# Performance work log

Hardware: AMD Instinct MI355X
Metric: run time of the kernel (lower is better)

Reference implementation:

```python
import jax, jax.numpy as jnp
import numpy as np

V = 20000; FV = 2000; PV = 31
SE = 400; FE = 50; PE = 5; NE = 5
FR = FE + PE + NE  # 60, field_rep_embed_size
H = 512; HH = H // 2  # decoder hidden, encoder per-direction hidden
B = 32; T = 32; S = 100
TE = 300  # target_lookup dim (hardcoded in module)


def setup_inputs() -> dict:
    key = jax.random.key(0)
    ks = jax.random.split(key, 26)
    g = lambda k, shape, s: (jax.random.normal(k, shape, jnp.float32) * s)
    inp = {}
    inp['sent'] = jax.random.randint(ks[0], (B, T), 0, V)
    inp['value'] = jax.random.randint(ks[1], (B, S), 0, V)
    inp['field'] = jax.random.randint(ks[2], (B, S), 0, FV)
    inp['ppos'] = jax.random.randint(ks[3], (B, S), 0, PV)
    inp['pneg'] = jax.random.randint(ks[4], (B, S), 0, PV)
    inp['batch_size'] = B
    inp['value_mask'] = jnp.ones((B, S), jnp.float32)
    inp['align_prob'] = jax.random.uniform(ks[5], (B, S, V), jnp.float32)
    # embedding tables
    inp['sent_emb'] = g(ks[6], (V, SE), 0.05)
    inp['field_emb'] = g(ks[7], (FV, FE), 0.05)
    inp['ppos_emb'] = g(ks[8], (PV, PE), 0.05)
    inp['pneg_emb'] = g(ks[9], (PV, NE), 0.05)
    inp['target_emb'] = g(ks[10], (V, TE), 0.05)
    # bidirectional encoder LSTM (per-direction hidden HH), torch gate order i,f,g,o
    ein = SE + FR
    inp['Wi_f'] = g(ks[11], (ein, 4 * HH), ein ** -0.5)
    inp['Wh_f'] = g(ks[12], (HH, 4 * HH), HH ** -0.5)
    inp['b_f'] = jnp.zeros((4 * HH,), jnp.float32)
    inp['Wi_b'] = g(ks[13], (ein, 4 * HH), ein ** -0.5)
    inp['Wh_b'] = g(ks[14], (HH, 4 * HH), HH ** -0.5)
    inp['b_b'] = jnp.zeros((4 * HH,), jnp.float32)
    # decoder LSTM cell + dual attention params
    inp['Wi_d'] = g(ks[15], (SE, 4 * H), SE ** -0.5)
    inp['Wh_d'] = g(ks[16], (H, 4 * H), H ** -0.5)
    inp['b_d'] = jnp.zeros((4 * H,), jnp.float32)
    inp['Wa'] = g(ks[17], (H, H), H ** -0.5)   # encoder-state attention proj
    inp['Wf'] = g(ks[18], (FR, H), FR ** -0.5) # field-rep attention proj
    inp['Wo'] = g(ks[19], (2 * H, H), (2 * H) ** -0.5)  # output proj [h;ctx]
    inp['Wl'] = g(ks[20], (2 * H + SE, 1), (2 * H + SE) ** -0.5)  # lamda gate
    inp['bl'] = jnp.zeros((1,), jnp.float32)
    # linear_out: encoder_hidden_size -> vocab
    inp['Wout'] = g(ks[21], (H, V), H ** -0.5)
    inp['bout'] = jnp.zeros((V,), jnp.float32)
    return inp


def _cell(x, h, c, Wi, Wh, b):
    z = x @ Wi + h @ Wh + b
    i, f, g, o = jnp.split(z, 4, axis=-1)
    c = jax.nn.sigmoid(f) * c + jax.nn.sigmoid(i) * jnp.tanh(g)
    h = jax.nn.sigmoid(o) * jnp.tanh(c)
    return h, c


def _run_lstm(xseq, Wi, Wh, b):
    # xseq [B,L,E] -> hs [B,L,Hn], (hT, cT)
    Bn = xseq.shape[0]; Hn = Wh.shape[0]
    init = (jnp.zeros((Bn, Hn), xseq.dtype), jnp.zeros((Bn, Hn), xseq.dtype))
    def step(carry, xt):
        h, c = _cell(xt, carry[0], carry[1], Wi, Wh, b)
        return (h, c), h
    (hT, cT), hs = jax.lax.scan(step, init, jnp.swapaxes(xseq, 0, 1))
    return jnp.swapaxes(hs, 0, 1), hT, cT


def reference(sent, value, field, ppos, pneg, batch_size, value_mask, align_prob,
              sent_emb, field_emb, ppos_emb, pneg_emb, target_emb,
              Wi_f, Wh_f, b_f, Wi_b, Wh_b, b_b,
              Wi_d, Wh_d, b_d, Wa, Wf, Wo, Wl, bl, Wout, bout):
    # --- encoder input: word emb of table values + field/pos/neg-pos embs ---
    input_d = sent_emb[value]                                     # [B,S,SE]
    input_z = jnp.concatenate([field_emb[field], ppos_emb[ppos], pneg_emb[pneg]], axis=2)  # [B,S,FR]
    enc_in = jnp.concatenate([input_d, input_z], axis=2)          # [B,S,SE+FR]
    # bidirectional LSTM (dropout is eval-mode identity)
    hs_f, hTf, cTf = _run_lstm(enc_in, Wi_f, Wh_f, b_f)
    hs_b, hTb, cTb = _run_lstm(enc_in[:, ::-1], Wi_b, Wh_b, b_b)
    enc_out = jnp.concatenate([hs_f, hs_b[:, ::-1]], axis=-1)     # [B,S,H]
    h0 = jnp.concatenate([hTf, hTb], axis=-1)                     # [B,H]
    c0 = jnp.concatenate([cTf, cTb], axis=-1)

    # --- dual-attention decoder ---
    x_seq = sent_emb[sent]                                        # [B,T,SE]
    enc_proj = jnp.einsum('bsh,hk->bsk', enc_out, Wa)             # word-level keys
    z_proj = jnp.einsum('bsf,fk->bsk', input_z, Wf)               # field-level keys

    def dstep(carry, xt):
        h, c = _cell(xt, carry[0], carry[1], Wi_d, Wh_d, b_d)
        alpha = jax.nn.softmax(jnp.einsum('bsh,bh->bs', enc_proj, h), axis=-1)
        beta = jax.nn.softmax(jnp.einsum('bsh,bh->bs', z_proj, h), axis=-1)
        g = alpha * beta
        g = g / (jnp.sum(g, axis=-1, keepdims=True) + 1e-9)       # dual attn weights
        ctx = jnp.einsum('bs,bsh->bh', g, enc_out)
        out = jnp.tanh(jnp.concatenate([h, ctx], axis=-1) @ Wo)   # [B,H]
        lam = jax.nn.sigmoid(jnp.concatenate([h, ctx, xt], axis=-1) @ Wl + bl)  # [B,1]
        return (h, c), (out, g, lam)

    (hT, cT), (outs, attn, lam) = jax.lax.scan(dstep, (h0, c0), jnp.swapaxes(x_seq, 0, 1))
    outs = jnp.swapaxes(outs, 0, 1)   # [B,T,H]
    attn = jnp.swapaxes(attn, 0, 1)   # [B,T,S]
    lam = jnp.swapaxes(lam, 0, 1)     # [B,T,1]

    p_mod = jax.nn.log_softmax(outs @ Wout + bout, axis=2)        # [B,T,V]
    p_lex = jnp.einsum('bts,bsv->btv', attn, align_prob)          # bmm
    p_bias = jax.nn.log_softmax(lam * p_lex + (1.0 - lam) * p_mod, axis=2)

    # position_idx_to_value: vectorized gather replacing the scalar double loop
    max_idx_attn = jnp.argmax(attn, axis=2)                       # [B,T]
    word_idx = jnp.take_along_axis(value, max_idx_attn, axis=1)   # [B,T]
    attn_pred = target_emb[word_idx]                              # [B,T,300]
    decoder_pred = target_emb[jnp.argmax(p_bias, axis=2)]         # [B,T,300]
    return p_bias, (hT, cT), attn_pred, decoder_pred
```

## Files before the change

### kernel.cpp

```cpp
#include <hip/hip_runtime.h>
#include <cstdint>
#include <cstddef>

static constexpr int Bn  = 32;
static constexpr int Tn  = 32;
static constexpr int Sn  = 100;
static constexpr int Vn  = 20000;
static constexpr int SEn = 400;
static constexpr int EINn= 460;
static constexpr int Hn  = 512;
static constexpr int HHn = 256;
static constexpr int TEn = 300;

__device__ __forceinline__ float sigm(float x) { return 1.f / (1.f + expf(-x)); }

__device__ __forceinline__ void fma4(float hk, const float4 w,
                                     float& zi, float& zf, float& zg, float& zo) {
    zi = fmaf(hk, w.x, zi); zf = fmaf(hk, w.y, zf);
    zg = fmaf(hk, w.z, zg); zo = fmaf(hk, w.w, zo);
}

__global__ __launch_bounds__(256) void embed_kernel(
    const int* __restrict__ value, const int* __restrict__ field,
    const int* __restrict__ ppos, const int* __restrict__ pneg,
    const int* __restrict__ sent,
    const float* __restrict__ sent_emb, const float* __restrict__ field_emb,
    const float* __restrict__ ppos_emb, const float* __restrict__ pneg_emb,
    float* __restrict__ enc_in, float* __restrict__ x_seq)
{
    int i = blockIdx.x * 256 + threadIdx.x;
    const int total1 = Bn * Sn * EINn;
    if (i < total1) {
        int e = i % EINn, bs = i / EINn;
        float v;
        if (e < SEn)      v = sent_emb[(size_t)value[bs] * SEn + e];
        else if (e < 450) v = field_emb[field[bs] * 50 + (e - 400)];
        else if (e < 455) v = ppos_emb[ppos[bs] * 5 + (e - 450)];
        else              v = pneg_emb[pneg[bs] * 5 + (e - 455)];
        enc_in[i] = v;
    } else {
        int i2 = i - total1;
        if (i2 < Bn * Tn * SEn) {
            int e = i2 % SEn, bt = i2 / SEn;
            x_seq[i2] = sent_emb[(size_t)sent[bt] * SEn + e];
        }
    }
}

__global__ __launch_bounds__(256) void transpose_wh_kernel(
    const float* __restrict__ Whf, const float* __restrict__ Whb,
    const float* __restrict__ Whd,
    float* __restrict__ Whf_t, float* __restrict__ Whb_t, float* __restrict__ Whd_t)
{
    int i = blockIdx.x * 256 + threadIdx.x;
    if (i < 65536) {
        int k = i >> 8, u = i & 255;
        const float* p = Whf + (size_t)k * 1024 + u;
        float4 o;
        o.x = p[0]; o.y = p[256]; o.z = p[512]; o.w = p[768];
        *(float4*)(Whf_t + (size_t)i * 4) = o;
        p = Whb + (size_t)k * 1024 + u;
        o.x = p[0]; o.y = p[256]; o.z = p[512]; o.w = p[768];
        *(float4*)(Whb_t + (size_t)i * 4) = o;
    } else {
        int j = i - 65536;
        if (j < 262144) {
            int k = j >> 9, u = j & 511;
            const float* p = Whd + (size_t)k * 2048 + u;
            float4 o;
            o.x = p[0]; o.y = p[512]; o.z = p[1024]; o.w = p[1536];
            *(float4*)(Whd_t + (size_t)j * 4) = o;
        }
    }
}

__global__ __launch_bounds__(256) void gemm128_kernel(
    const float* __restrict__ A, const float* __restrict__ Bm,
    const float* __restrict__ bias, float* __restrict__ C,
    int M, int N, int K, int lda, int ldb, int ldc)
{
    __shared__ float As[8][128];
    __shared__ float Bs[8][128];
    const int bm = blockIdx.y * 128, bn = blockIdx.x * 128;
    const int tid = threadIdx.x;
    const int tx = tid & 15, ty = tid >> 4;
    const int row0 = ty * 8, col0 = tx * 8;
    float acc[8][8] = {};
    for (int k0 = 0; k0 < K; k0 += 8) {
        #pragma unroll
        for (int i = 0; i < 4; ++i) {
            int idx = tid + 256 * i;
            int m = idx >> 3, kk = idx & 7;
            float v = 0.f;
            if (bm + m < M && k0 + kk < K) v = A[(size_t)(bm + m) * lda + (k0 + kk)];
            As[kk][m] = v;
        }
        #pragma unroll
        for (int i = 0; i < 4; ++i) {
            int idx = tid + 256 * i;
            int kk = idx >> 7, n = idx & 127;
            float v = 0.f;
            if (k0 + kk < K && bn + n < N) v = Bm[(size_t)(k0 + kk) * ldb + (bn + n)];
            Bs[kk][n] = v;
        }
        __syncthreads();
        #pragma unroll
        for (int kk = 0; kk < 8; ++kk) {
            float a[8], b[8];
            #pragma unroll
            for (int i = 0; i < 8; ++i) a[i] = As[kk][row0 + i];
            #pragma unroll
            for (int j = 0; j < 8; ++j) b[j] = Bs[kk][col0 + j];
            #pragma unroll
            for (int i = 0; i < 8; ++i)
                #pragma unroll
                for (int j = 0; j < 8; ++j) acc[i][j] = fmaf(a[i], b[j], acc[i][j]);
        }
        __syncthreads();
    }
    #pragma unroll
    for (int i = 0; i < 8; ++i) {
        int m = bm + row0 + i;
        if (m >= M) continue;
        #pragma unroll
        for (int j = 0; j < 8; ++j) {
            int n = bn + col0 + j;
            if (n < N) {
                float v = acc[i][j];
                if (bias) v += bias[n];
                C[(size_t)m * ldc + n] = v;
            }
        }
    }
}

__global__ __launch_bounds__(256) void enc_lstm2_kernel(
    const float* __restrict__ Xf, const float* __restrict__ Xb,
    const float4* __restrict__ Whf_t, const float4* __restrict__ Whb_t,
    float* __restrict__ enc_out, float* __restrict__ h0, float* __restrict__ c0)
{
    const int b = blockIdx.x >> 1, dir = blockIdx.x & 1;
    const float* __restrict__ X = dir ? Xb : Xf;
    const float4* __restrict__ W = dir ? Whb_t : Whf_t;
    __shared__ __align__(16) float h_sh[HHn];
    const int u = threadIdx.x;
    float c = 0.f;
    h_sh[u] = 0.f;
    __syncthreads();
    for (int step = 0; step < Sn; ++step) {
        const int s = dir ? (Sn - 1 - step) : step;
        const float* xr = X + ((size_t)(b * Sn + s)) * 1024;
        float zi = xr[u], zf = xr[256 + u], zg = xr[512 + u], zo = xr[768 + u];
        #pragma unroll 4
        for (int k4 = 0; k4 < 64; ++k4) {
            const float4 hv = *(const float4*)&h_sh[k4 << 2];
            const float4 w0 = W[((k4 << 2) + 0) * 256 + u];
            const float4 w1 = W[((k4 << 2) + 1) * 256 + u];
            const float4 w2 = W[((k4 << 2) + 2) * 256 + u];
            const float4 w3 = W[((k4 << 2) + 3) * 256 + u];
            fma4(hv.x, w0, zi, zf, zg, zo);
            fma4(hv.y, w1, zi, zf, zg, zo);
            fma4(hv.z, w2, zi, zf, zg, zo);
            fma4(hv.w, w3, zi, zf, zg, zo);
        }
        c = sigm(zf) * c + sigm(zi) * tanhf(zg);
        float h = sigm(zo) * tanhf(c);
        __syncthreads();
        h_sh[u] = h;
        enc_out[((size_t)(b * Sn + s)) * Hn + dir * HHn + u] = h;
        if (step == Sn - 1) {
            h0[b * Hn + dir * HHn + u] = h;
            c0[b * Hn + dir * HHn + u] = c;
        }
        __syncthreads();
    }
}

__global__ __launch_bounds__(256) void dec_lstm2_kernel(
    const float* __restrict__ Xd, const float4* __restrict__ Whd_t,
    const float* __restrict__ h0, const float* __restrict__ c0,
    float* __restrict__ h_all, float* __restrict__ hT, float* __restrict__ cT,
    float* __restrict__ hbuf, int* __restrict__ bar)
{
    const int b = blockIdx.x >> 1;
    const int tid = threadIdx.x;
    const int u = ((blockIdx.x & 1) << 8) + tid;
    __shared__ __align__(16) float h_sh[Hn];
    h_sh[tid]       = h0[b * Hn + tid];
    h_sh[tid + 256] = h0[b * Hn + 256 + tid];
    float c = c0[b * Hn + u];
    __syncthreads();
    for (int t = 0; t < Tn; ++t) {
        const float* xr = Xd + ((size_t)(b * Tn + t)) * 2048;
        float zi = xr[u], zf = xr[512 + u], zg = xr[1024 + u], zo = xr[1536 + u];
        #pragma unroll 4
        for (int k4 = 0; k4 < 128; ++k4) {
            const float4 hv = *(const float4*)&h_sh[k4 << 2];
            const float4 w0 = Whd_t[((k4 << 2) + 0) * 512 + u];
            const float4 w1 = Whd_t[((k4 << 2) + 1) * 512 + u];
            const float4 w2 = Whd_t[((k4 << 2) + 2) * 512 + u];
            const float4 w3 = Whd_t[((k4 << 2) + 3) * 512 + u];
            fma4(hv.x, w0, zi, zf, zg, zo);
            fma4(hv.y, w1, zi, zf, zg, zo);
            fma4(hv.z, w2, zi, zf, zg, zo);
            fma4(hv.w, w3, zi, zf, zg, zo);
        }
        c = sigm(zf) * c + sigm(zi) * tanhf(zg);
        float h = sigm(zo) * tanhf(c);
        h_all[((size_t)(b * Tn + t)) * Hn + u] = h;
        if (t == Tn - 1) { hT[b * Hn + u] = h; cT[b * Hn + u] = c; }
        __hip_atomic_store(&hbuf[b * Hn + u], h, __ATOMIC_RELEASE, __HIP_MEMORY_SCOPE_AGENT);
        __syncthreads();
        if (t == Tn - 1) break;
        if (tid == 0) {
            __hip_atomic_fetch_add(bar, 1, __ATOMIC_ACQ_REL, __HIP_MEMORY_SCOPE_AGENT);
            const int target = 64 * (t + 1);
            while (__hip_atomic_load(bar, __ATOMIC_ACQUIRE, __HIP_MEMORY_SCOPE_AGENT) < target)
                __builtin_amdgcn_s_sleep(8);
        }
        __syncthreads();
        h_sh[tid]       = __hip_atomic_load(&hbuf[b * Hn + tid],       __ATOMIC_ACQUIRE, __HIP_MEMORY_SCOPE_AGENT);
        h_sh[tid + 256] = __hip_atomic_load(&hbuf[b * Hn + 256 + tid], __ATOMIC_ACQUIRE, __HIP_MEMORY_SCOPE_AGENT);
        __syncthreads();
    }
}

__global__ __launch_bounds__(256) void dec_post_kernel(
    const float* __restrict__ h_all, const float* __restrict__ enc_proj,
    const float* __restrict__ z_proj, const float* __restrict__ enc_out,
    const float* __restrict__ x_seq, const float* __restrict__ Wo,
    const float* __restrict__ Wl, const float* __restrict__ bl,
    const int* __restrict__ value, const float* __restrict__ target_emb,
    float* __restrict__ outs, float* __restrict__ gattn,
    float* __restrict__ lamv, float* __restrict__ attn_pred)
{
    const int bt = blockIdx.x, b = bt >> 5;
    const int tid = threadIdx.x;
    __shared__ float h_sh[Hn];
    __shared__ float sc[2 * Sn];
    __shared__ float g_sh[Sn];
    __shared__ float ctx_sh[Hn];
    __shared__ float red[256];
    __shared__ int smax_sh;

    for (int i = tid; i < Hn; i += 256) h_sh[i] = h_all[(size_t)bt * Hn + i];
    __syncthreads();

    const int wave = tid >> 6, lane = tid & 63;
    for (int s = wave; s < Sn; s += 4) {
        const float* ep = enc_proj + ((size_t)b * Sn + s) * Hn;
        const float* zp = z_proj  + ((size_t)b * Sn + s) * Hn;
        float da = 0.f, db = 0.f;
        for (int j = lane; j < Hn; j += 64) {
            float hv = h_sh[j];
            da = fmaf(ep[j], hv, da);
            db = fmaf(zp[j], hv, db);
        }
        #pragma unroll
        for (int off = 32; off; off >>= 1) {
            da += __shfl_down(da, off);
            db += __shfl_down(db, off);
        }
        if (lane == 0) { sc[s] = da; sc[Sn + s] = db; }
    }
    __syncthreads();

    if (tid == 0) {
        float ma = -1e30f, mb = -1e30f;
        for (int s = 0; s < Sn; ++s) { ma = fmaxf(ma, sc[s]); mb = fmaxf(mb, sc[Sn + s]); }
        float sa = 0.f, sb = 0.f;
        for (int s = 0; s < Sn; ++s) {
            float ea = expf(sc[s] - ma), eb = expf(sc[Sn + s] - mb);
            sc[s] = ea; sc[Sn + s] = eb; sa += ea; sb += eb;
        }
        float gs = 0.f;
        for (int s = 0; s < Sn; ++s) { float g = (sc[s] / sa) * (sc[Sn + s] / sb); g_sh[s] = g; gs += g; }
        float inv = 1.f / (gs + 1e-9f);
        float best = -1.f; int bi = 0;
        for (int s = 0; s < Sn; ++s) {
            float g = g_sh[s] * inv; g_sh[s] = g;
            if (g > best) { best = g; bi = s; }
        }
        smax_sh = bi;
    }
    __syncthreads();

    for (int s = tid; s < Sn; s += 256) gattn[(size_t)bt * Sn + s] = g_sh[s];
    const int word = value[b * Sn + smax_sh];
    for (int e = tid; e < TEn; e += 256)
        attn_pred[(size_t)bt * TEn + e] = target_emb[(size_t)word * TEn + e];

    for (int u = tid; u < Hn; u += 256) {
        float acc = 0.f;
        for (int s = 0; s < Sn; ++s)
            acc = fmaf(g_sh[s], enc_out[((size_t)b * Sn + s) * Hn + u], acc);
        ctx_sh[u] = acc;
    }
    __syncthreads();

    for (int j = tid; j < Hn; j += 256) {
        float acc = 0.f;
        for (int k = 0; k < Hn; ++k) acc = fmaf(h_sh[k], Wo[(size_t)k * Hn + j], acc);
        for (int k = 0; k < Hn; ++k) acc = fmaf(ctx_sh[k], Wo[(size_t)(Hn + k) * Hn + j], acc);
        outs[(size_t)bt * Hn + j] = tanhf(acc);
    }

    float part = 0.f;
    for (int k = tid; k < Hn; k += 256) part = fmaf(h_sh[k], Wl[k], part);
    for (int k = tid; k < Hn; k += 256) part = fmaf(ctx_sh[k], Wl[Hn + k], part);
    const float* xr = x_seq + (size_t)bt * SEn;
    for (int k = tid; k < SEn; k += 256) part = fmaf(xr[k], Wl[2 * Hn + k], part);
    red[tid] = part;
    __syncthreads();
    for (int s2 = 128; s2; s2 >>= 1) {
        if (tid < s2) red[tid] += red[tid + s2];
        __syncthreads();
    }
    if (tid == 0) lamv[bt] = 1.f / (1.f + expf(-(red[0] + bl[0])));
}

__global__ __launch_bounds__(256) void p_lex_kernel(
    const float* __restrict__ gattn, const float* __restrict__ align_prob,
    float* __restrict__ p_lex)
{
    const int b = blockIdx.z, th = blockIdx.y, vc = blockIdx.x;
    const int tid = threadIdx.x;
    __shared__ float gT[Sn][17];
    for (int i = tid; i < Sn * 16; i += 256) {
        int s = i >> 4, tt = i & 15;
        gT[s][tt] = gattn[((size_t)(b * Tn + th * 16 + tt)) * Sn + s];
    }
    __syncthreads();
    const int v0 = vc * 1024 + tid * 4;
    if (v0 >= Vn) return;
    float acc[16][4] = {};
    for (int s = 0; s < Sn; ++s) {
        const float4 a = *(const float4*)(align_prob + ((size_t)b * Sn + s) * Vn + v0);
        #pragma unroll
        for (int tt = 0; tt < 16; ++tt) {
            float g = gT[s][tt];
            acc[tt][0] = fmaf(g, a.x, acc[tt][0]);
            acc[tt][1] = fmaf(g, a.y, acc[tt][1]);
            acc[tt][2] = fmaf(g, a.z, acc[tt][2]);
            acc[tt][3] = fmaf(g, a.w, acc[tt][3]);
        }
    }
    #pragma unroll
    for (int tt = 0; tt < 16; ++tt) {
        float4 o;
        o.x = acc[tt][0]; o.y = acc[tt][1]; o.z = acc[tt][2]; o.w = acc[tt][3];
        *(float4*)(p_lex + ((size_t)(b * Tn + th * 16 + tt)) * Vn + v0) = o;
    }
}

__global__ __launch_bounds__(256) void reduce1_kernel(
    const float* __restrict__ z, float* __restrict__ lse1)
{
    const int r = blockIdx.x, tid = threadIdx.x;
    const float* row = z + (size_t)r * Vn;
    __shared__ float red[256];
    float m = -1e30f;
    for (int v = tid; v < Vn; v += 256) m = fmaxf(m, row[v]);
    red[tid] = m; __syncthreads();
    for (int s = 128; s; s >>= 1) { if (tid < s) red[tid] = fmaxf(red[tid], red[tid + s]); __syncthreads(); }
    m = red[0]; __syncthreads();
    float sum = 0.f;
    for (int v = tid; v < Vn; v += 256) sum += expf(row[v] - m);
    red[tid] = sum; __syncthreads();
    for (int s = 128; s; s >>= 1) { if (tid < s) red[tid] += red[tid + s]; __syncthreads(); }
    if (tid == 0) lse1[r] = m + logf(red[0]);
}

__global__ __launch_bounds__(256) void combine_kernel(
    float* __restrict__ q, const float* __restrict__ p_lex,
    const float* __restrict__ lamv, const float* __restrict__ lse1,
    float* __restrict__ lse2, int* __restrict__ amax)
{
    const int r = blockIdx.x, tid = threadIdx.x;
    const float l = lamv[r], ls1 = lse1[r];
    float* row = q + (size_t)r * Vn;
    const float* pl = p_lex + (size_t)r * Vn;
    __shared__ float rm[256];
    __shared__ int ri[256];
    float m = -1e30f; int mi = 0;
    for (int v = tid; v < Vn; v += 256) {
        float qq = l * pl[v] + (1.f - l) * (row[v] - ls1);
        row[v] = qq;
        if (qq > m) { m = qq; mi = v; }
    }
    rm[tid] = m; ri[tid] = mi; __syncthreads();
    for (int s = 128; s; s >>= 1) {
        if (tid < s) {
            if (rm[tid + s] > rm[tid] || (rm[tid + s] == rm[tid] && ri[tid + s] < ri[tid])) {
                rm[tid] = rm[tid + s]; ri[tid] = ri[tid + s];
            }
        }
        __syncthreads();
    }
    m = rm[0];
    const int best = ri[0];
    __syncthreads();
    float sum = 0.f;
    for (int v = tid; v < Vn; v += 256) sum += expf(row[v] - m);
    rm[tid] = sum; __syncthreads();
    for (int s = 128; s; s >>= 1) { if (tid < s) rm[tid] += rm[tid + s]; __syncthreads(); }
    if (tid == 0) { lse2[r] = m + logf(rm[0]); amax[r] = best; }
}

__global__ __launch_bounds__(256) void finalize_kernel(
    float* __restrict__ pbias, const float* __restrict__ lse2,
    const int* __restrict__ amax, const float* __restrict__ target_emb,
    float* __restrict__ dec_pred)
{
    const int r = blockIdx.x, tid = threadIdx.x;
    const float ls = lse2[r];
    float* row = pbias + (size_t)r * Vn;
    for (int v = tid; v < Vn; v += 256) row[v] -= ls;
    const int wd = amax[r];
    for (int e = tid; e < TEn; e += 256)
        dec_pred[(size_t)r * TEn + e] = target_emb[(size_t)wd * TEn + e];
}

extern "C" void kernel_launch(void* const* d_in, const int* in_sizes, int n_in,
                              void* d_out, int out_size, void* d_ws, size_t ws_size,
                              hipStream_t stream)
{
    const int*   sent       = (const int*)d_in[0];
    const int*   value      = (const int*)d_in[1];
    const int*   field      = (const int*)d_in[2];
    const int*   ppos       = (const int*)d_in[3];
    const int*   pneg       = (const int*)d_in[4];
    const float* align_prob = (const float*)d_in[7];
    const float* sent_emb   = (const float*)d_in[8];
    const float* field_emb  = (const float*)d_in[9];
    const float* ppos_emb   = (const float*)d_in[10];
    const float* pneg_emb   = (const float*)d_in[11];
    const float* target_emb = (const float*)d_in[12];
    const float* Wi_f = (const float*)d_in[13];
    const float* Wh_f = (const float*)d_in[14];
    const float* b_f  = (const float*)d_in[15];
    const float* Wi_b = (const float*)d_in[16];
    const float* Wh_b = (const float*)d_in[17];
    const float* b_b  = (const float*)d_in[18];
    const float* Wi_d = (const float*)d_in[19];
    const float* Wh_d = (const float*)d_in[20];
    const float* b_d  = (const float*)d_in[21];
    const float* Wa   = (const float*)d_in[22];
    const float* Wf   = (const float*)d_in[23];
    const float* Wo   = (const float*)d_in[24];
    const float* Wl   = (const float*)d_in[25];
    const float* bl   = (const float*)d_in[26];
    const float* Wout = (const float*)d_in[27];
    const float* bout = (const float*)d_in[28];

    float* w = (float*)d_ws;
    float* enc_in   = w; w += (size_t)Bn * Sn * EINn;
    float* x_seq    = w; w += (size_t)Bn * Tn * SEn;
    float* Xf       = w; w += (size_t)Bn * Sn * 1024;
    float* Xb       = w; w += (size_t)Bn * Sn * 1024;
    float* Xd       = w; w += (size_t)Bn * Tn * 2048;
    float* enc_out  = w; w += (size_t)Bn * Sn * Hn;
    float* enc_proj = w; w += (size_t)Bn * Sn * Hn;
    float* z_proj   = w; w += (size_t)Bn * Sn * Hn;
    float* h0       = w; w += (size_t)Bn * Hn;
    float* c0       = w; w += (size_t)Bn * Hn;
    float* h_all    = w; w += (size_t)Bn * Tn * Hn;
    float* outs     = w; w += (size_t)Bn * Tn * Hn;
    float* gattn    = w; w += (size_t)Bn * Tn * Sn;
    float* lamv     = w; w += (size_t)Bn * Tn;
    float* p_lex    = w; w += (size_t)Bn * Tn * Vn;
    float* lse1     = w; w += (size_t)Bn * Tn;
    float* lse2     = w; w += (size_t)Bn * Tn;
    int*   amax     = (int*)w;

    float* Whf_t = p_lex;
    float* Whb_t = p_lex + 262144;
    float* Whd_t = p_lex + 524288;
    float* hbuf  = p_lex + 2000000;
    int*   bar   = (int*)(p_lex + 2100000);

    float* outp      = (float*)d_out;
    float* pbias     = outp;
    float* hT        = outp + (size_t)20480000;
    float* cT        = hT + Bn * Hn;
    float* attn_pred = cT + Bn * Hn;
    float* dec_pred  = attn_pred + (size_t)Bn * Tn * TEn;

    embed_kernel<<<7350, 256, 0, stream>>>(value, field, ppos, pneg, sent,
        sent_emb, field_emb, ppos_emb, pneg_emb, enc_in, x_seq);
    transpose_wh_kernel<<<1280, 256, 0, stream>>>(Wh_f, Wh_b, Wh_d, Whf_t, Whb_t, Whd_t);

    dim3 gXf(8, 25);
    gemm128_kernel<<<gXf, 256, 0, stream>>>(enc_in, Wi_f, b_f, Xf, 3200, 1024, 460, 460, 1024, 1024);
    gemm128_kernel<<<gXf, 256, 0, stream>>>(enc_in, Wi_b, b_b, Xb, 3200, 1024, 460, 460, 1024, 1024);
    dim3 gXd(16, 8);
    gemm128_kernel<<<gXd, 256, 0, stream>>>(x_seq, Wi_d, b_d, Xd, 1024, 2048, 400, 400, 2048, 2048);

    enc_lstm2_kernel<<<64, 256, 0, stream>>>(Xf, Xb, (const float4*)Whf_t,
        (const float4*)Whb_t, enc_out, h0, c0);

    dim3 gPr(4, 25);
    gemm128_kernel<<<gPr, 256, 0, stream>>>(enc_out, Wa, nullptr, enc_proj, 3200, 512, 512, 512, 512, 512);
    gemm128_kernel<<<gPr, 256, 0, stream>>>(enc_in + 400, Wf, nullptr, z_proj, 3200, 512, 60, 460, 512, 512);

    hipMemsetAsync(bar, 0, 64, stream);
    {
        void* args[] = { (void*)&Xd, (void*)&Whd_t, (void*)&h0, (void*)&c0,
                         (void*)&h_all, (void*)&hT, (void*)&cT,
                         (void*)&hbuf, (void*)&bar };
        hipLaunchCooperativeKernel((const void*)dec_lstm2_kernel,
                                   dim3(64), dim3(256), args, 0, stream);
    }

    dec_post_kernel<<<1024, 256, 0, stream>>>(h_all, enc_proj, z_proj, enc_out, x_seq,
        Wo, Wl, bl, value, target_emb, outs, gattn, lamv, attn_pred);

    dim3 gBig(157, 8);
    gemm128_kernel<<<gBig, 256, 0, stream>>>(outs, Wout, bout, pbias, 1024, 20000, 512, 512, 20000, 20000);

    dim3 gPl(20, 2, 32);
    p_lex_kernel<<<gPl, 256, 0, stream>>>(gattn, align_prob, p_lex);

    reduce1_kernel<<<1024, 256, 0, stream>>>(pbias, lse1);
    combine_kernel<<<1024, 256, 0, stream>>>(pbias, p_lex, lamv, lse1, lse2, amax);
    finalize_kernel<<<1024, 256, 0, stream>>>(pbias, lse2, amax, target_emb, dec_pred);

    (void)in_sizes; (void)n_in; (void)out_size; (void)ws_size;
}
```

Before: 4.184 ms.

## Repartition LSTM recurrences by hidden unit with grid barriers across all batches

Both encoder and decoder recurrent kernels now assign each block 8 hidden units for all 32 batch rows, so each weight column is loaded once per step and reused across the batch instead of every block streaming the whole recurrent weight matrix. Hidden state is exchanged via a double-buffered global buffer in unit-major layout with a cooperative grid barrier per step. This adds ~100 grid-wide synchronizations in the encoder and global-memory reads of h in place of shared memory.

```diff
diff --git a/kernel.cpp b/kernel.cpp
--- a/kernel.cpp
+++ b/kernel.cpp
@@ -18,6 +18,11 @@
                                      float& zi, float& zf, float& zg, float& zo) {
     zi = fmaf(hk, w.x, zi); zf = fmaf(hk, w.y, zf);
     zg = fmaf(hk, w.z, zg); zo = fmaf(hk, w.w, zo);
+}
+
+__device__ __forceinline__ void grid_wait(int* bar, int target) {
+    while (__hip_atomic_load(bar, __ATOMIC_ACQUIRE, __HIP_MEMORY_SCOPE_AGENT) < target)
+        __builtin_amdgcn_s_sleep(2);
 }
 
 __global__ __launch_bounds__(256) void embed_kernel(
@@ -134,94 +139,100 @@
     }
 }
 
-__global__ __launch_bounds__(256) void enc_lstm2_kernel(
+__global__ __launch_bounds__(256, 1) void enc_lstm4_kernel(
     const float* __restrict__ Xf, const float* __restrict__ Xb,
     const float4* __restrict__ Whf_t, const float4* __restrict__ Whb_t,
-    float* __restrict__ enc_out, float* __restrict__ h0, float* __restrict__ c0)
-{
-    const int b = blockIdx.x >> 1, dir = blockIdx.x & 1;
-    const float* __restrict__ X = dir ? Xb : Xf;
+    float* __restrict__ enc_out, float* __restrict__ h0t, float* __restrict__ c0t,
+    float* __restrict__ hbuf, int* __restrict__ bar)
+{
+    const int bb  = blockIdx.x;
+    const int dir = bb >> 5;
+    const int U0  = (bb & 31) * 8;
+    const float*  __restrict__ X = dir ? Xb : Xf;
     const float4* __restrict__ W = dir ? Whb_t : Whf_t;
-    __shared__ __align__(16) float h_sh[HHn];
-    const int u = threadIdx.x;
+    float* hb = hbuf + dir * 16384;
+    const int tid = threadIdx.x;
+    const int b = tid & 31, uu = tid >> 5;
+    const int unit = U0 + uu;
+    const float4* __restrict__ wcol = W + unit;
     float c = 0.f;
-    h_sh[u] = 0.f;
-    __syncthreads();
-    for (int step = 0; step < Sn; ++step) {
-        const int s = dir ? (Sn - 1 - step) : step;
-        const float* xr = X + ((size_t)(b * Sn + s)) * 1024;
-        float zi = xr[u], zf = xr[256 + u], zg = xr[512 + u], zo = xr[768 + u];
-        #pragma unroll 4
-        for (int k4 = 0; k4 < 64; ++k4) {
-            const float4 hv = *(const float4*)&h_sh[k4 << 2];
-            const float4 w0 = W[((k4 << 2) + 0) * 256 + u];
-            const float4 w1 = W[((k4 << 2) + 1) * 256 + u];
-            const float4 w2 = W[((k4 << 2) + 2) * 256 + u];
-            const float4 w3 = W[((k4 << 2) + 3) * 256 + u];
-            fma4(hv.x, w0, zi, zf, zg, zo);
-            fma4(hv.y, w1, zi, zf, zg, zo);
-            fma4(hv.z, w2, zi, zf, zg, zo);
-            fma4(hv.w, w3, zi, zf, zg, zo);
+
+    for (int s = 0; s < Sn; ++s) {
+        const int src_s = dir ? (Sn - 1 - s) : s;
+        const float* xr = X + ((size_t)(b * Sn + src_s)) * 1024 + unit;
+        float zi = xr[0], zf = xr[256], zg = xr[512], zo = xr[768];
+        if (s > 0) {
+            if (tid == 0) grid_wait(bar, 64 * s);
+            __syncthreads();
+            const float* hsrc = hb + ((s - 1) & 1) * 8192 + b;
+            #pragma unroll 8
+            for (int k = 0; k < 256; ++k) {
+                const float hv = __hip_atomic_load(&hsrc[k * 32],
+                                   __ATOMIC_RELAXED, __HIP_MEMORY_SCOPE_AGENT);
+                fma4(hv, wcol[(size_t)k * 256], zi, zf, zg, zo);
+            }
         }
         c = sigm(zf) * c + sigm(zi) * tanhf(zg);
-        float h = sigm(zo) * tanhf(c);
-        __syncthreads();
-        h_sh[u] = h;
-        enc_out[((size_t)(b * Sn + s)) * Hn + dir * HHn + u] = h;
-        if (step == Sn - 1) {
-            h0[b * Hn + dir * HHn + u] = h;
-            c0[b * Hn + dir * HHn + u] = c;
-        }
-        __syncthreads();
-    }
-}
-
-__global__ __launch_bounds__(256) void dec_lstm2_kernel(
+        const float h = sigm(zo) * tanhf(c);
+        enc_out[((size_t)(b * Sn + src_s)) * Hn + dir * HHn + unit] = h;
+        if (s == Sn - 1) {
+            h0t[(dir * HHn + unit) * 32 + b] = h;
+            c0t[(dir * HHn + unit) * 32 + b] = c;
+        } else {
+            __hip_atomic_store(&hb[(s & 1) * 8192 + unit * 32 + b], h,
+                               __ATOMIC_RELEASE, __HIP_MEMORY_SCOPE_AGENT);
+            __syncthreads();
+            if (tid == 0)
+                __hip_atomic_fetch_add(bar, 1, __ATOMIC_ACQ_REL, __HIP_MEMORY_SCOPE_AGENT);
+        }
+    }
+}
+
+__global__ __launch_bounds__(256, 1) void dec_lstm4_kernel(
     const float* __restrict__ Xd, const float4* __restrict__ Whd_t,
-    const float* __restrict__ h0, const float* __restrict__ c0,
+    const float* __restrict__ h0t, const float* __restrict__ c0t,
     float* __restrict__ h_all, float* __restrict__ hT, float* __restrict__ cT,
     float* __restrict__ hbuf, int* __restrict__ bar)
 {
-    const int b = blockIdx.x >> 1;
+    const int U0 = blockIdx.x * 8;
     const int tid = threadIdx.x;
-    const int u = ((blockIdx.x & 1) << 8) + tid;
-    __shared__ __align__(16) float h_sh[Hn];
-    h_sh[tid]       = h0[b * Hn + tid];
-    h_sh[tid + 256] = h0[b * Hn + 256 + tid];
-    float c = c0[b * Hn + u];
-    __syncthreads();
+    const int b = tid & 31, uu = tid >> 5;
+    const int unit = U0 + uu;
+    const float4* __restrict__ wcol = Whd_t + unit;
+    float c = c0t[unit * 32 + b];
+
     for (int t = 0; t < Tn; ++t) {
-        const float* xr = Xd + ((size_t)(b * Tn + t)) * 2048;
-        float zi = xr[u], zf = xr[512 + u], zg = xr[1024 + u], zo = xr[1536 + u];
-        #pragma unroll 4
-        for (int k4 = 0; k4 < 128; ++k4) {
-            const float4 hv = *(const float4*)&h_sh[k4 << 2];
-            const float4 w0 = Whd_t[((k4 << 2) + 0) * 512 + u];
-            const float4 w1 = Whd_t[((k4 << 2) + 1) * 512 + u];
-            const float4 w2 = Whd_t[((k4 << 2) + 2) * 512 + u];
-            const float4 w3 = Whd_t[((k4 << 2) + 3) * 512 + u];
-            fma4(hv.x, w0, zi, zf, zg, zo);
-            fma4(hv.y, w1, zi, zf, zg, zo);
-            fma4(hv.z, w2, zi, zf, zg, zo);
-            fma4(hv.w, w3, zi, zf, zg, zo);
+        const float* xr = Xd + ((size_t)(b * Tn + t)) * 2048 + unit;
+        float zi = xr[0], zf = xr[512], zg = xr[1024], zo = xr[1536];
+        if (t == 0) {
+            const float* hsrc = h0t + b;
+            #pragma unroll 8
+            for (int k = 0; k < 512; ++k)
+                fma4(hsrc[k * 32], wcol[(size_t)k * 512], zi, zf, zg, zo);
+        } else {
+            if (tid == 0) grid_wait(bar, 64 * t);
+            __syncthreads();
+            const float* hsrc = hbuf + ((t - 1) & 1) * 16384 + b;
+            #pragma unroll 8
+            for (int k = 0; k < 512; ++k) {
+                const float hv = __hip_atomic_load(&hsrc[k * 32],
+                                   __ATOMIC_RELAXED, __HIP_MEMORY_SCOPE_AGENT);
+                fma4(hv, wcol[(size_t)k * 512], zi, zf, zg, zo);
+            }
         }
         c = sigm(zf) * c + sigm(zi) * tanhf(zg);
-        float h = sigm(zo) * tanhf(c);
-        h_all[((size_t)(b * Tn + t)) * Hn + u] = h;
-        if (t == Tn - 1) { hT[b * Hn + u] = h; cT[b * Hn + u] = c; }
-        __hip_atomic_store(&hbuf[b * Hn + u], h, __ATOMIC_RELEASE, __HIP_MEMORY_SCOPE_AGENT);
-        __syncthreads();
-        if (t == Tn - 1) break;
-        if (tid == 0) {
-            __hip_atomic_fetch_add(bar, 1, __ATOMIC_ACQ_REL, __HIP_MEMORY_SCOPE_AGENT);
-            const int target = 64 * (t + 1);
-            while (__hip_atomic_load(bar, __ATOMIC_ACQUIRE, __HIP_MEMORY_SCOPE_AGENT) < target)
-                __builtin_amdgcn_s_sleep(8);
-        }
-        __syncthreads();
-        h_sh[tid]       = __hip_atomic_load(&hbuf[b * Hn + tid],       __ATOMIC_ACQUIRE, __HIP_MEMORY_SCOPE_AGENT);
-        h_sh[tid + 256] = __hip_atomic_load(&hbuf[b * Hn + 256 + tid], __ATOMIC_ACQUIRE, __HIP_MEMORY_SCOPE_AGENT);
-        __syncthreads();
+        const float h = sigm(zo) * tanhf(c);
+        h_all[((size_t)(b * Tn + t)) * Hn + unit] = h;
+        if (t == Tn - 1) {
+            hT[b * Hn + unit] = h;
+            cT[b * Hn + unit] = c;
+        } else {
+            __hip_atomic_store(&hbuf[(t & 1) * 16384 + unit * 32 + b], h,
+                               __ATOMIC_RELEASE, __HIP_MEMORY_SCOPE_AGENT);
+            __syncthreads();
+            if (tid == 0)
+                __hip_atomic_fetch_add(bar, 1, __ATOMIC_ACQ_REL, __HIP_MEMORY_SCOPE_AGENT);
+        }
     }
 }
 
@@ -462,8 +473,8 @@
     float* enc_out  = w; w += (size_t)Bn * Sn * Hn;
     float* enc_proj = w; w += (size_t)Bn * Sn * Hn;
     float* z_proj   = w; w += (size_t)Bn * Sn * Hn;
-    float* h0       = w; w += (size_t)Bn * Hn;
-    float* c0       = w; w += (size_t)Bn * Hn;
+    float* h0t      = w; w += (size_t)Bn * Hn;
+    float* c0t      = w; w += (size_t)Bn * Hn;
     float* h_all    = w; w += (size_t)Bn * Tn * Hn;
     float* outs     = w; w += (size_t)Bn * Tn * Hn;
     float* gattn    = w; w += (size_t)Bn * Tn * Sn;
@@ -473,11 +484,13 @@
     float* lse2     = w; w += (size_t)Bn * Tn;
     int*   amax     = (int*)w;
 
-    float* Whf_t = p_lex;
-    float* Whb_t = p_lex + 262144;
-    float* Whd_t = p_lex + 524288;
-    float* hbuf  = p_lex + 2000000;
-    int*   bar   = (int*)(p_lex + 2100000);
+    float* Whf_t  = p_lex;
+    float* Whb_t  = p_lex + 262144;
+    float* Whd_t  = p_lex + 524288;
+    float* hbuf_d = p_lex + 1600000;
+    float* hbuf_e = p_lex + 1700000;
+    int*   bar_e  = (int*)(p_lex + 1800000);
+    int*   bar_d  = bar_e + 64;
 
     float* outp      = (float*)d_out;
     float* pbias     = outp;
@@ -486,9 +499,14 @@
     float* attn_pred = cT + Bn * Hn;
     float* dec_pred  = attn_pred + (size_t)Bn * Tn * TEn;
 
+    const float4* Whf_t4 = (const float4*)Whf_t;
+    const float4* Whb_t4 = (const float4*)Whb_t;
+    const float4* Whd_t4 = (const float4*)Whd_t;
+
     embed_kernel<<<7350, 256, 0, stream>>>(value, field, ppos, pneg, sent,
         sent_emb, field_emb, ppos_emb, pneg_emb, enc_in, x_seq);
     transpose_wh_kernel<<<1280, 256, 0, stream>>>(Wh_f, Wh_b, Wh_d, Whf_t, Whb_t, Whd_t);
+    hipMemsetAsync(bar_e, 0, 512, stream);
 
     dim3 gXf(8, 25);
     gemm128_kernel<<<gXf, 256, 0, stream>>>(enc_in, Wi_f, b_f, Xf, 3200, 1024, 460, 460, 1024, 1024);
@@ -496,19 +514,23 @@
     dim3 gXd(16, 8);
     gemm128_kernel<<<gXd, 256, 0, stream>>>(x_seq, Wi_d, b_d, Xd, 1024, 2048, 400, 400, 2048, 2048);
 
-    enc_lstm2_kernel<<<64, 256, 0, stream>>>(Xf, Xb, (const float4*)Whf_t,
-        (const float4*)Whb_t, enc_out, h0, c0);
+    {
+        void* args[] = { (void*)&Xf, (void*)&Xb, (void*)&Whf_t4, (void*)&Whb_t4,
+                         (void*)&enc_out, (void*)&h0t, (void*)&c0t,
+                         (void*)&hbuf_e, (void*)&bar_e };
+        hipLaunchCooperativeKernel((const void*)enc_lstm4_kernel,
+                                   dim3(64), dim3(256), args, 0, stream);
+    }
 
     dim3 gPr(4, 25);
     gemm128_kernel<<<gPr, 256, 0, stream>>>(enc_out, Wa, nullptr, enc_proj, 3200, 512, 512, 512, 512, 512);
     gemm128_kernel<<<gPr, 256, 0, stream>>>(enc_in + 400, Wf, nullptr, z_proj, 3200, 512, 60, 460, 512, 512);
 
-    hipMemsetAsync(bar, 0, 64, stream);
     {
-        void* args[] = { (void*)&Xd, (void*)&Whd_t, (void*)&h0, (void*)&c0,
+        void* args[] = { (void*)&Xd, (void*)&Whd_t4, (void*)&h0t, (void*)&c0t,
                          (void*)&h_all, (void*)&hT, (void*)&cT,
-                         (void*)&hbuf, (void*)&bar };
-        hipLaunchCooperativeKernel((const void*)dec_lstm2_kernel,
+                         (void*)&hbuf_d, (void*)&bar_d };
+        hipLaunchCooperativeKernel((const void*)dec_lstm4_kernel,
                                    dim3(64), dim3(256), args, 0, stream);
     }
 
```

Measured after the change: 5.495 ms. 31.3% more time.
